# Kernel tuning notes

Measured on AMD Instinct MI355X. Metric: run time of the kernel, lower is better.

## Reference

```python
import jax, jax.numpy as jnp
import numpy as np

DIM = 128
HEADS = 4
HEAD_DIM = DIM // HEADS
WS = (8, 8)
N = WS[0] * WS[1]
B = 4096
SCALE = HEAD_DIM ** -0.5


def _relative_position_index():
    # Swin-style relative position index, [N, N] int
    ch = np.arange(WS[0]); cw = np.arange(WS[1])
    coords = np.stack(np.meshgrid(ch, cw, indexing='ij'))          # [2, ws0, ws1]
    flat = coords.reshape(2, -1)                                    # [2, N]
    rel = flat[:, :, None] - flat[:, None, :]                       # [2, N, N]
    rel = rel.transpose(1, 2, 0)                                    # [N, N, 2]
    rel[:, :, 0] += WS[0] - 1
    rel[:, :, 1] += WS[1] - 1
    rel[:, :, 0] *= 2 * WS[1] - 1
    return jnp.asarray(rel.sum(-1))

REL_IDX = _relative_position_index()


def setup_inputs() -> dict:
    key = jax.random.key(0)
    ks = jax.random.split(key, 16)
    def lin(k, din, dout):
        return jax.random.normal(k, (din, dout), jnp.float32) * (din ** -0.5)
    return {
        'x': jax.random.normal(ks[0], (B, N, DIM), jnp.float32),
        'f': jax.random.normal(ks[1], (B, N, DIM), jnp.float32),
        'wq': lin(ks[2], DIM, DIM), 'bq': jnp.zeros((DIM,), jnp.float32),
        'wkv': lin(ks[3], DIM, 2 * DIM), 'bkv': jnp.zeros((2 * DIM,), jnp.float32),
        'wq_f': lin(ks[4], DIM, DIM), 'bq_f': jnp.zeros((DIM,), jnp.float32),
        'wkv_f': lin(ks[5], DIM, 2 * DIM), 'bkv_f': jnp.zeros((2 * DIM,), jnp.float32),
        'bias_table': jax.random.normal(ks[6], ((2 * WS[0] - 1) * (2 * WS[1] - 1), HEADS), jnp.float32) * 0.02,
        'wproj': lin(ks[7], DIM, DIM), 'bproj': jnp.zeros((DIM,), jnp.float32),
    }


def _qkv(t, wq, bq, wkv, bkv):
    Bn, Nn, C = t.shape
    q = (t @ wq + bq).reshape(Bn, Nn, HEADS, HEAD_DIM).transpose(0, 2, 1, 3)   # [B,H,N,D]
    kv = (t @ wkv + bkv).reshape(Bn, Nn, 2, HEADS, HEAD_DIM).transpose(2, 0, 3, 1, 4)
    return q, kv[0], kv[1]


def reference(x, f, wq, bq, wkv, bkv, wq_f, bq_f, wkv_f, bkv_f, bias_table, wproj, bproj):
    q, k, v = _qkv(x, wq, bq, wkv, bkv)
    attn = jnp.einsum('bhnd,bhmd->bhnm', q * SCALE, k)              # [B,H,N,N]
    q_f, k_f, _ = _qkv(f, wq_f, bq_f, wkv_f, bkv_f)
    attn_f = jnp.einsum('bhnd,bhmd->bhnm', q_f * SCALE, k_f)

    bias = bias_table[REL_IDX.reshape(-1)].reshape(N, N, HEADS)     # gather
    bias = bias.transpose(2, 0, 1)                                   # [H,N,N]
    ratio = attn.shape[-1] // bias.shape[-1]
    if ratio > 1:  # repeat last axis (no-op here since N == ws0*ws1)
        bias = jnp.repeat(bias, ratio, axis=-1)

    attn = (attn + bias[None]) * (attn_f + bias[None])               # joint modulation
    attn = jax.nn.softmax(attn, axis=-1)
    out = jnp.einsum('bhnm,bhmd->bhnd', attn, v)                     # [B,H,N,D]
    out = out.transpose(0, 2, 1, 3).reshape(x.shape[0], N, DIM)
    return out @ wproj + bproj
```

## Files before the change

### kernel.cpp

```cpp
#include <hip/hip_runtime.h>

typedef unsigned short u16;
typedef _Float16  f16x8  __attribute__((ext_vector_type(8)));
typedef _Float16  f16x4  __attribute__((ext_vector_type(4)));
typedef float     f32x4  __attribute__((ext_vector_type(4)));

#define MFMA_F16(a,b,c)  __builtin_amdgcn_mfma_f32_16x16x32_f16(a,b,c,0,0,0)

#define NTOK 64
#define DIM_ 128
#define SCALE_ 0.17677669529663687f

#define HREG 6464
#define KOFF 2176
#define VOFF 4352
#define SQK  34
#define SP   68
#define SAO  36
#define SVT  66
#define SMEM_U16 25856

__device__ __forceinline__ u16 f2h_u(float x) {
    _Float16 h = (_Float16)x;
    return __builtin_bit_cast(u16, h);
}

__global__ void wja_prep(const float* __restrict__ wq, const float* __restrict__ wkv,
                         const float* __restrict__ wq_f, const float* __restrict__ wkv_f,
                         const float* __restrict__ wproj, u16* __restrict__ ws)
{
    const int blk = blockIdx.x;
    const int l = threadIdx.x;
    const float* W; int ldw, colbase;
    if (blk < 32)       { W = wq;    ldw = 128; colbase = (blk      >> 2) * 16; }
    else if (blk < 96)  { W = wkv;   ldw = 256; colbase = ((blk- 32) >> 2) * 16; }
    else if (blk < 128) { W = wq_f;  ldw = 128; colbase = ((blk- 96) >> 2) * 16; }
    else if (blk < 160) { W = wkv_f; ldw = 256; colbase = ((blk-128) >> 2) * 16; }
    else                { W = wproj; ldw = 128; colbase = ((blk-160) >> 2) * 16; }
    const int ks = blk & 3;
    const int m = l & 15, g = l >> 4;
    u16* dst = ws + blk * 512 + l * 8;
    #pragma unroll
    for (int i = 0; i < 8; ++i)
        dst[i] = f2h_u(W[(size_t)(32*ks + 8*g + i) * ldw + colbase + m]);
}

__global__ __launch_bounds__(256, 2)
void wja_fused(
    const float* __restrict__ x, const float* __restrict__ f,
    const float* __restrict__ bq, const float* __restrict__ bkv,
    const float* __restrict__ bq_f, const float* __restrict__ bkv_f,
    const float* __restrict__ bproj, const float* __restrict__ btab,
    const u16* __restrict__ ws, float* __restrict__ out)
{
    __shared__ __align__(16) u16 smem[SMEM_U16];
    const int b    = blockIdx.x;
    const int tid  = threadIdx.x;
    const int w    = tid >> 6;
    const int lane = tid & 63;
    const int g    = lane >> 4;
    const int c    = lane & 15;
    const f32x4 zf4 = {0.f, 0.f, 0.f, 0.f};

    u16* const hb = smem + w * HREG;

    const float* const xb = x + (size_t)b * (NTOK * DIM_);
    const float* const fb = f + (size_t)b * (NTOK * DIM_);

    auto ldf16 = [](const float* p) -> f16x8 {
        f16x8 r;
        #pragma unroll
        for (int i = 0; i < 8; ++i) r[i] = (_Float16)p[i];
        return r;
    };
    auto ldlds8 = [](const u16* p) -> f16x8 {
        struct P2 { f16x4 lo, hi; } t;
        t.lo = *(const f16x4*)p;
        t.hi = *(const f16x4*)(p + 4);
        return __builtin_bit_cast(f16x8, t);
    };
    auto ldlds4 = [](const u16* p) -> f16x8 {
        struct P4 { unsigned a, b, c, d; } t;
        t.a = *(const unsigned*)(p);
        t.b = *(const unsigned*)(p + 2);
        t.c = *(const unsigned*)(p + 4);
        t.d = *(const unsigned*)(p + 6);
        return __builtin_bit_cast(f16x8, t);
    };

    f16x8 xfr[4], ffr[4];
    #pragma unroll
    for (int ks = 0; ks < 4; ++ks) {
        xfr[ks] = ldf16(xb + (16*w + c) * DIM_ + 32*ks + 8*g);
        ffr[ks] = ldf16(fb + (16*w + c) * DIM_ + 32*ks + 8*g);
    }

    auto gemmA = [&](const f16x8* afr, int wbase, const float* biasv, int which) {
        #pragma unroll
        for (int lct = 0; lct < 8; ++lct) {
            f32x4 acc = zf4;
            #pragma unroll
            for (int ks = 0; ks < 4; ++ks) {
                f16x8 bfr = *(const f16x8*)(ws + (wbase + 4*lct + ks) * 512 + lane * 8);
                acc = MFMA_F16(afr[ks], bfr, acc);
            }
            float bv = biasv[16*lct + c];
            const int hh = lct >> 1;
            const int cc = ((lct & 1) << 4) + c;
            #pragma unroll
            for (int i = 0; i < 4; ++i) {
                int row = 16*w + 4*g + i;
                u16 vv = f2h_u(acc[i] + bv);
                if (which == 0)      smem[hh*HREG + row*SQK + cc] = vv;
                else if (which == 1) smem[hh*HREG + KOFF + row*SQK + cc] = vv;
                else                 smem[hh*HREG + VOFF + cc*SVT + row] = vv;
            }
        }
    };

    gemmA(xfr,   0, bq,        0);
    gemmA(xfr,  32, bkv,       1);
    gemmA(xfr,  64, bkv + 128, 2);
    __syncthreads();

    f32x4 S[4][4];
    {
        f16x8 qfr[4], kfr[4];
        #pragma unroll
        for (int t = 0; t < 4; ++t) {
            qfr[t] = ldlds4(hb + (16*t + c) * SQK + 8*g);
            kfr[t] = ldlds4(hb + KOFF + (16*t + c) * SQK + 8*g);
        }
        #pragma unroll
        for (int mt = 0; mt < 4; ++mt)
            #pragma unroll
            for (int nt = 0; nt < 4; ++nt)
                S[mt][nt] = MFMA_F16(qfr[mt], kfr[nt], zf4);
    }
    __syncthreads();

    gemmA(ffr,  96, bq_f,  0);
    gemmA(ffr, 128, bkv_f, 1);
    __syncthreads();

    {
        f16x8 kfr[4];
        #pragma unroll
        for (int t = 0; t < 4; ++t)
            kfr[t] = ldlds4(hb + KOFF + (16*t + c) * SQK + 8*g);
        #pragma unroll
        for (int mt = 0; mt < 4; ++mt) {
            f16x8 qfr = ldlds4(hb + (16*mt + c) * SQK + 8*g);
            #pragma unroll
            for (int nt = 0; nt < 4; ++nt) {
                f32x4 sf = MFMA_F16(qfr, kfr[nt], zf4);
                int j = 16*nt + c;
                #pragma unroll
                for (int i = 0; i < 4; ++i) {
                    int r = 16*mt + 4*g + i;
                    int idx = ((r >> 3) - (j >> 3) + 7) * 15 + ((r & 7) - (j & 7) + 7);
                    float bv = btab[idx * 4 + w];
                    S[mt][nt][i] = (S[mt][nt][i] * SCALE_ + bv) * (sf[i] * SCALE_ + bv);
                }
            }
        }
    }

    float rmax[4][4], rinv[4][4];
    #pragma unroll
    for (int mt = 0; mt < 4; ++mt)
        #pragma unroll
        for (int i = 0; i < 4; ++i) {
            float m = fmaxf(fmaxf(S[mt][0][i], S[mt][1][i]), fmaxf(S[mt][2][i], S[mt][3][i]));
            #pragma unroll
            for (int d = 1; d < 16; d <<= 1) m = fmaxf(m, __shfl_xor(m, d));
            rmax[mt][i] = m;
        }
    #pragma unroll
    for (int mt = 0; mt < 4; ++mt)
        #pragma unroll
        for (int i = 0; i < 4; ++i) {
            float s0 = 0.f;
            #pragma unroll
            for (int nt = 0; nt < 4; ++nt) {
                float e = __expf(S[mt][nt][i] - rmax[mt][i]);
                S[mt][nt][i] = e;
                s0 += e;
            }
            #pragma unroll
            for (int d = 1; d < 16; d <<= 1) s0 += __shfl_xor(s0, d);
            rinv[mt][i] = 1.0f / s0;
        }

    #pragma unroll
    for (int mt = 0; mt < 4; ++mt)
        #pragma unroll
        for (int nt = 0; nt < 4; ++nt)
            #pragma unroll
            for (int i = 0; i < 4; ++i)
                hb[(16*mt + 4*g + i) * SP + 16*nt + c] = f2h_u(S[mt][nt][i] * rinv[mt][i]);

    f32x4 O[4][2] = { { zf4, zf4 }, { zf4, zf4 }, { zf4, zf4 }, { zf4, zf4 } };
    #pragma unroll
    for (int ks = 0; ks < 2; ++ks) {
        f16x8 pfr[4], vfr[2];
        #pragma unroll
        for (int mt = 0; mt < 4; ++mt)
            pfr[mt] = ldlds8(hb + (16*mt + c) * SP + 32*ks + 8*g);
        #pragma unroll
        for (int nt = 0; nt < 2; ++nt)
            vfr[nt] = ldlds4(hb + VOFF + (16*nt + c) * SVT + 32*ks + 8*g);
        #pragma unroll
        for (int mt = 0; mt < 4; ++mt)
            #pragma unroll
            for (int nt = 0; nt < 2; ++nt)
                O[mt][nt] = MFMA_F16(pfr[mt], vfr[nt], O[mt][nt]);
    }

    #pragma unroll
    for (int mt = 0; mt < 4; ++mt)
        #pragma unroll
        for (int nt = 0; nt < 2; ++nt)
            #pragma unroll
            for (int i = 0; i < 4; ++i)
                hb[(16*mt + 4*g + i) * SAO + 16*nt + c] = f2h_u(O[mt][nt][i]);

    __syncthreads();

    f32x4 PO[4][2] = { { zf4, zf4 }, { zf4, zf4 }, { zf4, zf4 }, { zf4, zf4 } };
    #pragma unroll
    for (int ks = 0; ks < 4; ++ks) {
        const u16* ao = smem + ks * HREG;
        f16x8 afr[4];
        #pragma unroll
        for (int mt = 0; mt < 4; ++mt)
            afr[mt] = ldlds8(ao + (16*mt + c) * SAO + 8*g);
        #pragma unroll
        for (int lct = 0; lct < 2; ++lct) {
            f16x8 bfr = *(const f16x8*)(ws + (160 + (2*w + lct) * 4 + ks) * 512 + lane * 8);
            #pragma unroll
            for (int mt = 0; mt < 4; ++mt)
                PO[mt][lct] = MFMA_F16(afr[mt], bfr, PO[mt][lct]);
        }
    }
    __syncthreads();

    float* const fin = (float*)smem;
    #pragma unroll
    for (int lct = 0; lct < 2; ++lct) {
        float bv = bproj[32*w + 16*lct + c];
        #pragma unroll
        for (int mt = 0; mt < 4; ++mt)
            #pragma unroll
            for (int i = 0; i < 4; ++i)
                fin[(16*mt + 4*g + i) * 132 + 32*w + 16*lct + c] = PO[mt][lct][i] + bv;
    }
    __syncthreads();

    {
        const int row = tid >> 2, cb = (tid & 3) * 32;
        float* gout = out + (size_t)b * 8192 + row * 128 + cb;
        const float* src = fin + row * 132 + cb;
        #pragma unroll
        for (int q2 = 0; q2 < 8; ++q2)
            *(f32x4*)(gout + q2 * 4) = *(const f32x4*)(src + q2 * 4);
    }
}

extern "C" void kernel_launch(void* const* d_in, const int* in_sizes, int n_in,
                              void* d_out, int out_size, void* d_ws, size_t ws_size,
                              hipStream_t stream)
{
    const float* x     = (const float*)d_in[0];
    const float* f     = (const float*)d_in[1];
    const float* wq    = (const float*)d_in[2];
    const float* bq    = (const float*)d_in[3];
    const float* wkv   = (const float*)d_in[4];
    const float* bkv   = (const float*)d_in[5];
    const float* wq_f  = (const float*)d_in[6];
    const float* bq_f  = (const float*)d_in[7];
    const float* wkv_f = (const float*)d_in[8];
    const float* bkv_f = (const float*)d_in[9];
    const float* btab  = (const float*)d_in[10];
    const float* wproj = (const float*)d_in[11];
    const float* bproj = (const float*)d_in[12];
    u16* ws    = (u16*)d_ws;
    float* out = (float*)d_out;

    hipLaunchKernelGGL(wja_prep, dim3(192), dim3(64), 0, stream,
                       wq, wkv, wq_f, wkv_f, wproj, ws);
    hipLaunchKernelGGL(wja_fused, dim3(4096), dim3(256), 0, stream,
                       x, f, bq, bkv, bq_f, bkv_f, bproj, btab, ws, out);
}
```

Measured before the change: 222.6 us.

## Precompute bias table, widen LDS loads, pack conversions, store output directly

Several independent changes. Shared-memory strides are padded so fragments can be read with wider 8-byte loads. Input fp32 loads are vectorised and packed into fp16 with cvt_pkrtz. V stores are packed. The relative-position bias is pre-expanded into a dense per-head 64x64 table in workspace, removing the per-element index arithmetic. Softmax max and sum are merged into one loop. The final output is written straight from registers instead of staged through LDS. This trades two barriers and LDS traffic for less coalesced global stores, a larger LDS footprint and round-toward-zero fp16 rounding.

```diff
diff --git a/kernel.cpp b/kernel.cpp
--- a/kernel.cpp
+++ b/kernel.cpp
@@ -3,22 +3,26 @@
 typedef unsigned short u16;
 typedef _Float16  f16x8  __attribute__((ext_vector_type(8)));
 typedef _Float16  f16x4  __attribute__((ext_vector_type(4)));
+typedef _Float16  f16x2  __attribute__((ext_vector_type(2)));
 typedef float     f32x4  __attribute__((ext_vector_type(4)));
 
 #define MFMA_F16(a,b,c)  __builtin_amdgcn_mfma_f32_16x16x32_f16(a,b,c,0,0,0)
+#define PKRTZ(a,b) __builtin_bit_cast(f16x2, __builtin_amdgcn_cvt_pkrtz((a),(b)))
 
 #define NTOK 64
 #define DIM_ 128
 #define SCALE_ 0.17677669529663687f
 
-#define HREG 6464
-#define KOFF 2176
-#define VOFF 4352
-#define SQK  34
-#define SP   68
-#define SAO  36
-#define SVT  66
-#define SMEM_U16 25856
+#define HREG 6784
+#define KOFF 2304
+#define VOFF 4608
+#define SQK  36
+#define SP   72
+#define SAO  40
+#define SVT  68
+#define SMEM_U16 27136
+
+#define WS_TAB_F32 49152
 
 __device__ __forceinline__ u16 f2h_u(float x) {
     _Float16 h = (_Float16)x;
@@ -27,22 +31,33 @@
 
 __global__ void wja_prep(const float* __restrict__ wq, const float* __restrict__ wkv,
                          const float* __restrict__ wq_f, const float* __restrict__ wkv_f,
-                         const float* __restrict__ wproj, u16* __restrict__ ws)
+                         const float* __restrict__ wproj, const float* __restrict__ btab,
+                         u16* __restrict__ ws)
 {
     const int blk = blockIdx.x;
     const int l = threadIdx.x;
-    const float* W; int ldw, colbase;
-    if (blk < 32)       { W = wq;    ldw = 128; colbase = (blk      >> 2) * 16; }
-    else if (blk < 96)  { W = wkv;   ldw = 256; colbase = ((blk- 32) >> 2) * 16; }
-    else if (blk < 128) { W = wq_f;  ldw = 128; colbase = ((blk- 96) >> 2) * 16; }
-    else if (blk < 160) { W = wkv_f; ldw = 256; colbase = ((blk-128) >> 2) * 16; }
-    else                { W = wproj; ldw = 128; colbase = ((blk-160) >> 2) * 16; }
-    const int ks = blk & 3;
-    const int m = l & 15, g = l >> 4;
-    u16* dst = ws + blk * 512 + l * 8;
-    #pragma unroll
-    for (int i = 0; i < 8; ++i)
-        dst[i] = f2h_u(W[(size_t)(32*ks + 8*g + i) * ldw + colbase + m]);
+    if (blk < 192) {
+        const float* W; int ldw, colbase;
+        if (blk < 32)       { W = wq;    ldw = 128; colbase = (blk      >> 2) * 16; }
+        else if (blk < 96)  { W = wkv;   ldw = 256; colbase = ((blk- 32) >> 2) * 16; }
+        else if (blk < 128) { W = wq_f;  ldw = 128; colbase = ((blk- 96) >> 2) * 16; }
+        else if (blk < 160) { W = wkv_f; ldw = 256; colbase = ((blk-128) >> 2) * 16; }
+        else                { W = wproj; ldw = 128; colbase = ((blk-160) >> 2) * 16; }
+        const int ks = blk & 3;
+        const int m = l & 15, g = l >> 4;
+        u16* dst = ws + blk * 512 + l * 8;
+        #pragma unroll
+        for (int i = 0; i < 8; ++i)
+            dst[i] = f2h_u(W[(size_t)(32*ks + 8*g + i) * ldw + colbase + m]);
+    } else {
+        const int h = blk - 192;
+        float* tab = (float*)ws + WS_TAB_F32 + h * 4096;
+        for (int e = l; e < 4096; e += 64) {
+            int r = e >> 6, j = e & 63;
+            int idx = ((r >> 3) - (j >> 3) + 7) * 15 + ((r & 7) - (j & 7) + 7);
+            tab[e] = btab[idx * 4 + h];
+        }
+    }
 }
 
 __global__ __launch_bounds__(256, 2)
@@ -51,7 +66,7 @@
     const float* __restrict__ bq, const float* __restrict__ bkv,
     const float* __restrict__ bq_f, const float* __restrict__ bkv_f,
     const float* __restrict__ bproj, const float* __restrict__ btab,
-    const u16* __restrict__ ws, float* __restrict__ out)
+    const u16* __restrict__ ws, float* __restrict__ out, int use_tab)
 {
     __shared__ __align__(16) u16 smem[SMEM_U16];
     const int b    = blockIdx.x;
@@ -68,10 +83,14 @@
     const float* const fb = f + (size_t)b * (NTOK * DIM_);
 
     auto ldf16 = [](const float* p) -> f16x8 {
-        f16x8 r;
-        #pragma unroll
-        for (int i = 0; i < 8; ++i) r[i] = (_Float16)p[i];
-        return r;
+        f32x4 v0 = *(const f32x4*)p;
+        f32x4 v1 = *(const f32x4*)(p + 4);
+        struct Q { f16x2 a, b, c, d; } t;
+        t.a = PKRTZ(v0[0], v0[1]);
+        t.b = PKRTZ(v0[2], v0[3]);
+        t.c = PKRTZ(v1[0], v1[1]);
+        t.d = PKRTZ(v1[2], v1[3]);
+        return __builtin_bit_cast(f16x8, t);
     };
     auto ldlds8 = [](const u16* p) -> f16x8 {
         struct P2 { f16x4 lo, hi; } t;
@@ -79,14 +98,6 @@
         t.hi = *(const f16x4*)(p + 4);
         return __builtin_bit_cast(f16x8, t);
     };
-    auto ldlds4 = [](const u16* p) -> f16x8 {
-        struct P4 { unsigned a, b, c, d; } t;
-        t.a = *(const unsigned*)(p);
-        t.b = *(const unsigned*)(p + 2);
-        t.c = *(const unsigned*)(p + 4);
-        t.d = *(const unsigned*)(p + 6);
-        return __builtin_bit_cast(f16x8, t);
-    };
 
     f16x8 xfr[4], ffr[4];
     #pragma unroll
@@ -107,13 +118,17 @@
             float bv = biasv[16*lct + c];
             const int hh = lct >> 1;
             const int cc = ((lct & 1) << 4) + c;
-            #pragma unroll
-            for (int i = 0; i < 4; ++i) {
-                int row = 16*w + 4*g + i;
-                u16 vv = f2h_u(acc[i] + bv);
-                if (which == 0)      smem[hh*HREG + row*SQK + cc] = vv;
-                else if (which == 1) smem[hh*HREG + KOFF + row*SQK + cc] = vv;
-                else                 smem[hh*HREG + VOFF + cc*SVT + row] = vv;
+            if (which == 2) {
+                struct H4 { f16x2 lo, hi; } t;
+                t.lo = PKRTZ(acc[0] + bv, acc[1] + bv);
+                t.hi = PKRTZ(acc[2] + bv, acc[3] + bv);
+                *(f16x4*)(smem + hh*HREG + VOFF + cc*SVT + 16*w + 4*g) =
+                    __builtin_bit_cast(f16x4, t);
+            } else {
+                const int base = hh*HREG + (which ? KOFF : 0);
+                #pragma unroll
+                for (int i = 0; i < 4; ++i)
+                    smem[base + (16*w + 4*g + i)*SQK + cc] = f2h_u(acc[i] + bv);
             }
         }
     };
@@ -128,8 +143,8 @@
         f16x8 qfr[4], kfr[4];
         #pragma unroll
         for (int t = 0; t < 4; ++t) {
-            qfr[t] = ldlds4(hb + (16*t + c) * SQK + 8*g);
-            kfr[t] = ldlds4(hb + KOFF + (16*t + c) * SQK + 8*g);
+            qfr[t] = ldlds8(hb + (16*t + c) * SQK + 8*g);
+            kfr[t] = ldlds8(hb + KOFF + (16*t + c) * SQK + 8*g);
         }
         #pragma unroll
         for (int mt = 0; mt < 4; ++mt)
@@ -144,13 +159,14 @@
     __syncthreads();
 
     {
+        const float* tab = (const float*)ws + WS_TAB_F32 + w * 4096;
         f16x8 kfr[4];
         #pragma unroll
         for (int t = 0; t < 4; ++t)
-            kfr[t] = ldlds4(hb + KOFF + (16*t + c) * SQK + 8*g);
+            kfr[t] = ldlds8(hb + KOFF + (16*t + c) * SQK + 8*g);
         #pragma unroll
         for (int mt = 0; mt < 4; ++mt) {
-            f16x8 qfr = ldlds4(hb + (16*mt + c) * SQK + 8*g);
+            f16x8 qfr = ldlds8(hb + (16*mt + c) * SQK + 8*g);
             #pragma unroll
             for (int nt = 0; nt < 4; ++nt) {
                 f32x4 sf = MFMA_F16(qfr, kfr[nt], zf4);
@@ -158,15 +174,20 @@
                 #pragma unroll
                 for (int i = 0; i < 4; ++i) {
                     int r = 16*mt + 4*g + i;
-                    int idx = ((r >> 3) - (j >> 3) + 7) * 15 + ((r & 7) - (j & 7) + 7);
-                    float bv = btab[idx * 4 + w];
+                    float bv;
+                    if (use_tab) {
+                        bv = tab[r * 64 + j];
+                    } else {
+                        int idx = ((r >> 3) - (j >> 3) + 7) * 15 + ((r & 7) - (j & 7) + 7);
+                        bv = btab[idx * 4 + w];
+                    }
                     S[mt][nt][i] = (S[mt][nt][i] * SCALE_ + bv) * (sf[i] * SCALE_ + bv);
                 }
             }
         }
     }
 
-    float rmax[4][4], rinv[4][4];
+    float rinv[4][4];
     #pragma unroll
     for (int mt = 0; mt < 4; ++mt)
         #pragma unroll
@@ -174,16 +195,10 @@
             float m = fmaxf(fmaxf(S[mt][0][i], S[mt][1][i]), fmaxf(S[mt][2][i], S[mt][3][i]));
             #pragma unroll
             for (int d = 1; d < 16; d <<= 1) m = fmaxf(m, __shfl_xor(m, d));
-            rmax[mt][i] = m;
-        }
-    #pragma unroll
-    for (int mt = 0; mt < 4; ++mt)
-        #pragma unroll
-        for (int i = 0; i < 4; ++i) {
             float s0 = 0.f;
             #pragma unroll
             for (int nt = 0; nt < 4; ++nt) {
-                float e = __expf(S[mt][nt][i] - rmax[mt][i]);
+                float e = __expf(S[mt][nt][i] - m);
                 S[mt][nt][i] = e;
                 s0 += e;
             }
@@ -206,10 +221,10 @@
         f16x8 pfr[4], vfr[2];
         #pragma unroll
         for (int mt = 0; mt < 4; ++mt)
-            pfr[mt] = ldlds8(hb + (16*mt + c) * SP + 32*ks + 8*g);
+            pfr[mt] = *(const f16x8*)(hb + (16*mt + c) * SP + 32*ks + 8*g);
         #pragma unroll
         for (int nt = 0; nt < 2; ++nt)
-            vfr[nt] = ldlds4(hb + VOFF + (16*nt + c) * SVT + 32*ks + 8*g);
+            vfr[nt] = ldlds8(hb + VOFF + (16*nt + c) * SVT + 32*ks + 8*g);
         #pragma unroll
         for (int mt = 0; mt < 4; ++mt)
             #pragma unroll
@@ -234,7 +249,7 @@
         f16x8 afr[4];
         #pragma unroll
         for (int mt = 0; mt < 4; ++mt)
-            afr[mt] = ldlds8(ao + (16*mt + c) * SAO + 8*g);
+            afr[mt] = *(const f16x8*)(ao + (16*mt + c) * SAO + 8*g);
         #pragma unroll
         for (int lct = 0; lct < 2; ++lct) {
             f16x8 bfr = *(const f16x8*)(ws + (160 + (2*w + lct) * 4 + ks) * 512 + lane * 8);
@@ -243,9 +258,8 @@
                 PO[mt][lct] = MFMA_F16(afr[mt], bfr, PO[mt][lct]);
         }
     }
-    __syncthreads();
-
-    float* const fin = (float*)smem;
+
+    float* const ob = out + (size_t)b * 8192;
     #pragma unroll
     for (int lct = 0; lct < 2; ++lct) {
         float bv = bproj[32*w + 16*lct + c];
@@ -253,17 +267,7 @@
         for (int mt = 0; mt < 4; ++mt)
             #pragma unroll
             for (int i = 0; i < 4; ++i)
-                fin[(16*mt + 4*g + i) * 132 + 32*w + 16*lct + c] = PO[mt][lct][i] + bv;
-    }
-    __syncthreads();
-
-    {
-        const int row = tid >> 2, cb = (tid & 3) * 32;
-        float* gout = out + (size_t)b * 8192 + row * 128 + cb;
-        const float* src = fin + row * 132 + cb;
-        #pragma unroll
-        for (int q2 = 0; q2 < 8; ++q2)
-            *(f32x4*)(gout + q2 * 4) = *(const f32x4*)(src + q2 * 4);
+                ob[(16*mt + 4*g + i) * 128 + 32*w + 16*lct + c] = PO[mt][lct][i] + bv;
     }
 }
 
@@ -287,8 +291,9 @@
     u16* ws    = (u16*)d_ws;
     float* out = (float*)d_out;
 
-    hipLaunchKernelGGL(wja_prep, dim3(192), dim3(64), 0, stream,
-                       wq, wkv, wq_f, wkv_f, wproj, ws);
+    const int use_tab = (ws_size >= 262144) ? 1 : 0;
+    hipLaunchKernelGGL(wja_prep, dim3(use_tab ? 196 : 192), dim3(64), 0, stream,
+                       wq, wkv, wq_f, wkv_f, wproj, btab, ws);
     hipLaunchKernelGGL(wja_fused, dim3(4096), dim3(256), 0, stream,
-                       x, f, bq, bkv, bq_f, bkv_f, bproj, btab, ws, out);
-}
+                       x, f, bq, bkv, bq_f, bkv_f, bproj, btab, ws, out, use_tab);
+}
```

After: 419.1 us. 1.88x slower.
